# Performance work log

Hardware: AMD Instinct MI355X
Metric: run time of the kernel (lower is better)

## Reference

```python
import jax, jax.numpy as jnp
import numpy as np

N = 100_000   # nodes
E = 800_000   # edges
F_IN = 128    # num_features
E_IN = 64     # edge_dim
H = 100       # n_hidden
L = 2         # num_gnn_layers
BN_EPS = 1e-5


def _lin(key, fan_in, fan_out, extra=()):
    kw, _ = jax.random.split(key)
    w = jax.random.normal(kw, (*extra, fan_in, fan_out), jnp.float32) / np.float32(np.sqrt(fan_in))
    b = jnp.zeros((*extra, fan_out), jnp.float32)
    return w, b


def setup_inputs() -> dict:
    key = jax.random.key(0)
    ks = jax.random.split(key, 12)
    x = jax.random.normal(ks[0], (N, F_IN), jnp.float32)
    edge_index = jax.random.randint(ks[1], (2, E), 0, N, dtype=jnp.int32)
    edge_attr = jax.random.normal(ks[2], (E, E_IN), jnp.float32)
    node_w, node_b = _lin(ks[3], F_IN, H)
    edge_w, edge_b = _lin(ks[4], E_IN, H)
    lin_w, lin_b = _lin(ks[5], H, H, (L,))   # GINEConv edge lin per layer
    w1, b1 = _lin(ks[6], H, H, (L,))         # GINEConv nn first Linear
    w2, b2 = _lin(ks[7], H, H, (L,))         # GINEConv nn second Linear
    gamma = jnp.ones((L, H), jnp.float32)
    beta = jnp.zeros((L, H), jnp.float32)
    ew1, eb1 = _lin(ks[8], 3 * H, H, (L,))   # edge-update MLP
    ew2, eb2 = _lin(ks[9], H, H, (L,))
    mw1, mb1 = _lin(ks[10], 3 * H, 50)
    k11, k12 = jax.random.split(ks[11])
    mw2, mb2 = _lin(k11, 50, 25)
    mw3, mb3 = _lin(k12, 25, 2)
    return dict(x=x, edge_index=edge_index, edge_attr=edge_attr,
                node_w=node_w, node_b=node_b, edge_w=edge_w, edge_b=edge_b,
                lin_w=lin_w, lin_b=lin_b, w1=w1, b1=b1, w2=w2, b2=b2,
                gamma=gamma, beta=beta, ew1=ew1, eb1=eb1, ew2=ew2, eb2=eb2,
                mw1=mw1, mb1=mb1, mw2=mw2, mb2=mb2, mw3=mw3, mb3=mb3)


def reference(x, edge_index, edge_attr, node_w, node_b, edge_w, edge_b,
              lin_w, lin_b, w1, b1, w2, b2, gamma, beta,
              ew1, eb1, ew2, eb2, mw1, mb1, mw2, mb2, mw3, mb3):
    src, dst = edge_index[0], edge_index[1]
    h = x @ node_w + node_b          # [N, H]
    e = edge_attr @ edge_w + edge_b  # [E, H]
    for i in range(L):
        # GINEConv: message = relu(x_src + lin(edge_attr)); sum-aggregate at dst
        msg = jax.nn.relu(h[src] + (e @ lin_w[i] + lin_b[i]))       # [E, H]
        agg = jax.ops.segment_sum(msg, dst, num_segments=N)         # [N, H]
        z = h + agg                                                  # (1+eps)*x + aggr, eps=0
        z = jax.nn.relu(z @ w1[i] + b1[i]) @ w2[i] + b2[i]
        # BatchNorm over nodes (training mode, biased variance)
        mu = z.mean(0)
        var = z.var(0)
        z = (z - mu) * jax.lax.rsqrt(var + BN_EPS) * gamma[i] + beta[i]
        h = (h + jax.nn.relu(z)) / 2
        # edge update: emlp(cat(x_src, x_dst, e))
        cat = jnp.concatenate([h[src], h[dst], e], axis=-1)         # [E, 3H]
        e = e + (jax.nn.relu(cat @ ew1[i] + eb1[i]) @ ew2[i] + eb2[i]) / 2
    feat = jnp.concatenate(
        [jax.nn.relu(jnp.concatenate([h[src], h[dst]], axis=-1)), e], axis=1)  # [E, 3H]
    out = jax.nn.relu(feat @ mw1 + mb1)
    out = jax.nn.relu(out @ mw2 + mb2)
    return out @ mw3 + mb3  # [E, 2]
```

## Files before the change

kernel.cpp:

```cpp
#include <hip/hip_runtime.h>

#define N_NODES 100000
#define N_EDGES 800000
#define HDIM 100
#define LDP 112
#define TSTR 104

typedef __attribute__((ext_vector_type(8))) short bf16x8;
typedef __attribute__((ext_vector_type(4))) float f32x4;

__device__ inline uint packsplit(float v) {
    uint u = __float_as_uint(v);
    float r = v - __uint_as_float(u & 0xFFFF0000u);
    return (u & 0xFFFF0000u) | (__float_as_uint(r) >> 16);
}
__device__ inline float recw(uint w) {
    return __uint_as_float(w & 0xFFFF0000u) + __uint_as_float(w << 16);
}
__device__ inline uint4 relu4(uint4 a) {
    a.x &= ~(uint)((int)a.x >> 31); a.y &= ~(uint)((int)a.y >> 31);
    a.z &= ~(uint)((int)a.z >> 31); a.w &= ~(uint)((int)a.w >> 31);
    return a;
}
__device__ inline void unpack16(uint4 a, uint4 b, bf16x8& h8, bf16x8& l8) {
    union { uint u[4]; bf16x8 v; } H, L;
    H.u[0] = __builtin_amdgcn_perm(a.y, a.x, 0x07060302u);
    H.u[1] = __builtin_amdgcn_perm(a.w, a.z, 0x07060302u);
    H.u[2] = __builtin_amdgcn_perm(b.y, b.x, 0x07060302u);
    H.u[3] = __builtin_amdgcn_perm(b.w, b.z, 0x07060302u);
    L.u[0] = __builtin_amdgcn_perm(a.y, a.x, 0x05040100u);
    L.u[1] = __builtin_amdgcn_perm(a.w, a.z, 0x05040100u);
    L.u[2] = __builtin_amdgcn_perm(b.y, b.x, 0x05040100u);
    L.u[3] = __builtin_amdgcn_perm(b.w, b.z, 0x05040100u);
    h8 = H.v; l8 = L.v;
}
__device__ inline void split8(float4 a, float4 b, bf16x8& h8, bf16x8& l8) {
    float v[8] = {a.x, a.y, a.z, a.w, b.x, b.y, b.z, b.w};
    bf16x8 hh, ll;
#pragma unroll
    for (int i = 0; i < 8; ++i) {
        uint u = __float_as_uint(v[i]);
        hh[i] = (short)(u >> 16);
        float r = v[i] - __uint_as_float(u & 0xFFFF0000u);
        ll[i] = (short)(__float_as_uint(r) >> 16);
    }
    h8 = hh; l8 = ll;
}

template<int CONCAT>
__global__ __launch_bounds__(256)
void pack_k(const float* __restrict__ W, ushort* __restrict__ hi, ushort* __restrict__ lo,
            int K, int NC, int Kpad, int NCpad, int total)
{
    int idx = blockIdx.x * 256 + threadIdx.x;
    if (idx >= total) return;
    int per = NCpad * Kpad;
    int b = idx / per, rem = idx - b * per;
    int col = rem / Kpad, kv = rem - col * Kpad;
    int srck; bool valid;
    if (CONCAT) {
        int seg = kv >> 7, off = kv & 127;
        srck = seg * 100 + off;
        valid = (off < 100) && (srck < K) && (col < NC);
    } else {
        srck = kv;
        valid = (kv < K) && (col < NC);
    }
    float v = valid ? W[(long)b * K * NC + (long)srck * NC + col] : 0.f;
    uint w = packsplit(v);
    hi[idx] = (ushort)(w >> 16);
    lo[idx] = (ushort)(w & 0xFFFFu);
}

template<int TILES, int TPW, int STEPS, int MODE, int GATHER, int AFP32, int OUTF32, int CLAMP>
__global__ __launch_bounds__(256, 2)
void gemm9_k(const uint* aP, int lda, const float* __restrict__ aF, int ldaf,
             const ushort* __restrict__ wH, const ushort* __restrict__ wL,
             const float* __restrict__ bias,
             float* __restrict__ Cf, uint* cP, int ldc,
             int M, int NC, const int* __restrict__ g0)
{
    constexpr int KPADW = STEPS * 32;
    const int tid  = threadIdx.x;
    const int lane = tid & 63;
    const int w    = tid >> 6;
    const int cl   = lane & 15;
    const int kgrp = lane >> 4;
    const long row0 = (long)blockIdx.x * 64;

    int arows[4];
#pragma unroll
    for (int rg = 0; rg < 4; ++rg) {
        long grow = row0 + rg * 16 + cl;
        int gc = (int)((grow < M) ? grow : (M - 1));
        arows[rg] = (GATHER == 3) ? g0[gc] : gc;
    }

    uint4  aw0[2][4], aw1[2][4];
    float4 af0[2][4], af1[2][4];
    bf16x8 bh[2][TPW], bl[2][TPW];
    f32x4  acc[TPW][4];
#pragma unroll
    for (int tp = 0; tp < TPW; ++tp)
#pragma unroll
        for (int rg = 0; rg < 4; ++rg) acc[tp][rg] = (f32x4){0.f, 0.f, 0.f, 0.f};

    auto loadA = [&](int st, int sl) {
        const int kk = st * 32 + kgrp * 8;
#pragma unroll
        for (int rg = 0; rg < 4; ++rg) {
            if (AFP32) {
                const float* p = aF + (size_t)arows[rg] * ldaf + kk;
                af0[sl][rg] = *(const float4*)p;
                af1[sl][rg] = *(const float4*)(p + 4);
            } else {
                bool ok = !CLAMP || ((st & 3) != 3) || (kgrp == 0);
                if (ok) {
                    const uint* p = aP + (size_t)arows[rg] * lda + kk;
                    aw0[sl][rg] = *(const uint4*)p;
                    aw1[sl][rg] = *(const uint4*)(p + 4);
                } else {
                    aw0[sl][rg] = make_uint4(0, 0, 0, 0);
                    aw1[sl][rg] = make_uint4(0, 0, 0, 0);
                }
            }
        }
    };
    auto loadB = [&](int st, int sl) {
        int kk = st * 32 + kgrp * 8;
#pragma unroll
        for (int tp = 0; tp < TPW; ++tp) {
            int colw = (w * TPW + tp) * 16 + cl;
            bh[sl][tp] = *(const bf16x8*)(wH + (size_t)colw * KPADW + kk);
            bl[sl][tp] = *(const bf16x8*)(wL + (size_t)colw * KPADW + kk);
        }
    };

    loadA(0, 0); loadB(0, 0);
    if (STEPS > 1) { loadA(1, 1); loadB(1, 1); }

#pragma unroll
    for (int st = 0; st < STEPS; ++st) {
        const int sl = st & 1;
#pragma unroll
        for (int rg = 0; rg < 4; ++rg) {
            bf16x8 aH, aL;
            if (AFP32) split8(af0[sl][rg], af1[sl][rg], aH, aL);
            else       unpack16(aw0[sl][rg], aw1[sl][rg], aH, aL);
#pragma unroll
            for (int tp = 0; tp < TPW; ++tp) {
                acc[tp][rg] = __builtin_amdgcn_mfma_f32_16x16x32_bf16(aL, bh[sl][tp], acc[tp][rg], 0, 0, 0);
                acc[tp][rg] = __builtin_amdgcn_mfma_f32_16x16x32_bf16(aH, bl[sl][tp], acc[tp][rg], 0, 0, 0);
                acc[tp][rg] = __builtin_amdgcn_mfma_f32_16x16x32_bf16(aH, bh[sl][tp], acc[tp][rg], 0, 0, 0);
            }
        }
        if (st + 2 < STEPS) { loadA(st + 2, sl); loadB(st + 2, sl); }
    }

#pragma unroll
    for (int tp = 0; tp < TPW; ++tp) {
        int col = (w * TPW + tp) * 16 + cl;
        if (col >= NC) continue;
        float bv = bias[col];
#pragma unroll
        for (int rg = 0; rg < 4; ++rg) {
#pragma unroll
            for (int i = 0; i < 4; ++i) {
                long grow = row0 + rg * 16 + kgrp * 4 + i;
                if (grow >= M) continue;
                float v = acc[tp][rg][i] + bv;
                if (MODE == 1) v = fmaxf(v, 0.f);
                long o = grow * (long)ldc + col;
                if (OUTF32) Cf[o] = v;
                else        cP[o] = packsplit(v);
            }
        }
    }
}

__global__ __launch_bounds__(256, 2)
void msg_agg_k(const uint* __restrict__ eP,
               const ushort* __restrict__ wH, const ushort* __restrict__ wL,
               const float* __restrict__ bias,
               const uint* __restrict__ hP,
               const int* __restrict__ psrc, const int* __restrict__ pdst,
               float* __restrict__ aggF)
{
    __shared__ float sm[64 * 108];
    __shared__ int sd[64];
    const int tid = threadIdx.x, lane = tid & 63, w = tid >> 6;
    const int cl = lane & 15, kgrp = lane >> 4;
    const long row0 = (long)blockIdx.x * 64;

    if (tid < 64) sd[tid] = pdst[row0 + tid];

    int sr[4][4];
#pragma unroll
    for (int rg = 0; rg < 4; ++rg)
#pragma unroll
        for (int i = 0; i < 4; ++i)
            sr[rg][i] = psrc[row0 + rg * 16 + kgrp * 4 + i];

    uint4 aw0[2][4], aw1[2][4];
    bf16x8 bh[2][2], bl[2][2];
    f32x4 acc[2][4];
#pragma unroll
    for (int tp = 0; tp < 2; ++tp)
#pragma unroll
        for (int rg = 0; rg < 4; ++rg) acc[tp][rg] = (f32x4){0.f, 0.f, 0.f, 0.f};

    auto loadA = [&](int st, int sl) {
        const int kk = st * 32 + kgrp * 8;
        bool ok = ((st & 3) != 3) || (kgrp == 0);
#pragma unroll
        for (int rg = 0; rg < 4; ++rg) {
            if (ok) {
                const uint* p = eP + (size_t)(row0 + rg * 16 + cl) * LDP + kk;
                aw0[sl][rg] = *(const uint4*)p;
                aw1[sl][rg] = *(const uint4*)(p + 4);
            } else {
                aw0[sl][rg] = make_uint4(0, 0, 0, 0);
                aw1[sl][rg] = make_uint4(0, 0, 0, 0);
            }
        }
    };
    auto loadB = [&](int st, int sl) {
        int kk = st * 32 + kgrp * 8;
#pragma unroll
        for (int tp = 0; tp < 2; ++tp) {
            int colw = (w * 2 + tp) * 16 + cl;
            bh[sl][tp] = *(const bf16x8*)(wH + (size_t)colw * 128 + kk);
            bl[sl][tp] = *(const bf16x8*)(wL + (size_t)colw * 128 + kk);
        }
    };

    loadA(0, 0); loadB(0, 0); loadA(1, 1); loadB(1, 1);
#pragma unroll
    for (int st = 0; st < 4; ++st) {
        const int sl = st & 1;
#pragma unroll
        for (int rg = 0; rg < 4; ++rg) {
            bf16x8 aH, aL;
            unpack16(aw0[sl][rg], aw1[sl][rg], aH, aL);
#pragma unroll
            for (int tp = 0; tp < 2; ++tp) {
                acc[tp][rg] = __builtin_amdgcn_mfma_f32_16x16x32_bf16(aL, bh[sl][tp], acc[tp][rg], 0, 0, 0);
                acc[tp][rg] = __builtin_amdgcn_mfma_f32_16x16x32_bf16(aH, bl[sl][tp], acc[tp][rg], 0, 0, 0);
                acc[tp][rg] = __builtin_amdgcn_mfma_f32_16x16x32_bf16(aH, bh[sl][tp], acc[tp][rg], 0, 0, 0);
            }
        }
        if (st + 2 < 4) { loadA(st + 2, sl); loadB(st + 2, sl); }
    }

#pragma unroll
    for (int tp = 0; tp < 2; ++tp) {
        int col = (w * 2 + tp) * 16 + cl;
        if (col < 100) {
            float bv = bias[col];
#pragma unroll
            for (int rg = 0; rg < 4; ++rg)
#pragma unroll
                for (int i = 0; i < 4; ++i) {
                    int row = rg * 16 + kgrp * 4 + i;
                    float hv = recw(hP[(size_t)sr[rg][i] * LDP + col]);
                    sm[row * 108 + col] = fmaxf(acc[tp][rg][i] + bv + hv, 0.f);
                }
        }
    }
    __syncthreads();

    if (tid < 100) {
        const int c = tid;
        int cur = sd[0];
        float s = 0.f;
        bool first = true;
        for (int r = 0; r < 64; ++r) {
            int d = sd[r];
            if (d != cur) {
                bool contPrev = first && (row0 > 0) && (pdst[row0 - 1] == cur);
                if (contPrev) atomicAdd(&aggF[(size_t)cur * TSTR + c], s);
                else aggF[(size_t)cur * TSTR + c] = recw(hP[(size_t)cur * LDP + c]) + s;
                first = false; s = 0.f; cur = d;
            }
            s += sm[r * 108 + c];
        }
        bool contPrev = first && (row0 > 0) && (pdst[row0 - 1] == cur);
        bool contNext = (row0 + 64 < N_EDGES) && (pdst[row0 + 64] == cur);
        if (contPrev || contNext) atomicAdd(&aggF[(size_t)cur * TSTR + c], s);
        else aggF[(size_t)cur * TSTR + c] = recw(hP[(size_t)cur * LDP + c]) + s;
    }
}

__global__ __launch_bounds__(256, 2)
void fused_edge_k(const uint* __restrict__ hP, uint* eP,
                  const ushort* __restrict__ w1H, const ushort* __restrict__ w1L,
                  const float* __restrict__ b1v,
                  const ushort* __restrict__ w2H, const ushort* __restrict__ w2L,
                  const float* __restrict__ b2v,
                  const int* __restrict__ g0, const int* __restrict__ g1)
{
    __shared__ uint sm[64 * 108];
    const int tid = threadIdx.x, lane = tid & 63, w = tid >> 6;
    const int cl = lane & 15, kgrp = lane >> 4;
    const long row0 = (long)blockIdx.x * 64;

    int rs[4], rd[4];
#pragma unroll
    for (int rg = 0; rg < 4; ++rg) {
        long gr = row0 + rg * 16 + cl;
        rs[rg] = g0[gr]; rd[rg] = g1[gr];
    }

    uint4 aw0[2][4], aw1[2][4];
    bf16x8 bh[2][2], bl[2][2];
    f32x4 acc[2][4];
#pragma unroll
    for (int tp = 0; tp < 2; ++tp)
#pragma unroll
        for (int rg = 0; rg < 4; ++rg) acc[tp][rg] = (f32x4){0.f, 0.f, 0.f, 0.f};

    auto loadA = [&](int st, int sl) {
        int seg = st >> 2, inseg = (st & 3) * 32 + kgrp * 8;
        bool ok = ((st & 3) != 3) || (kgrp == 0);
        const uint* base = (seg == 2) ? eP : hP;
#pragma unroll
        for (int rg = 0; rg < 4; ++rg) {
            if (ok) {
                long row = (seg == 0) ? rs[rg] : (seg == 1) ? rd[rg] : (row0 + rg * 16 + cl);
                const uint* p = base + (size_t)row * LDP + inseg;
                aw0[sl][rg] = *(const uint4*)p;
                aw1[sl][rg] = *(const uint4*)(p + 4);
            } else {
                aw0[sl][rg] = make_uint4(0, 0, 0, 0);
                aw1[sl][rg] = make_uint4(0, 0, 0, 0);
            }
        }
    };
    auto loadB = [&](int st, int sl) {
        int kk = st * 32 + kgrp * 8;
#pragma unroll
        for (int tp = 0; tp < 2; ++tp) {
            int colw = (w * 2 + tp) * 16 + cl;
            bh[sl][tp] = *(const bf16x8*)(w1H + (size_t)colw * 384 + kk);
            bl[sl][tp] = *(const bf16x8*)(w1L + (size_t)colw * 384 + kk);
        }
    };

    loadA(0, 0); loadB(0, 0); loadA(1, 1); loadB(1, 1);
#pragma unroll
    for (int st = 0; st < 12; ++st) {
        const int sl = st & 1;
#pragma unroll
        for (int rg = 0; rg < 4; ++rg) {
            bf16x8 aH, aL;
            unpack16(aw0[sl][rg], aw1[sl][rg], aH, aL);
#pragma unroll
            for (int tp = 0; tp < 2; ++tp) {
                acc[tp][rg] = __builtin_amdgcn_mfma_f32_16x16x32_bf16(aL, bh[sl][tp], acc[tp][rg], 0, 0, 0);
                acc[tp][rg] = __builtin_amdgcn_mfma_f32_16x16x32_bf16(aH, bl[sl][tp], acc[tp][rg], 0, 0, 0);
                acc[tp][rg] = __builtin_amdgcn_mfma_f32_16x16x32_bf16(aH, bh[sl][tp], acc[tp][rg], 0, 0, 0);
            }
        }
        if (st + 2 < 12) { loadA(st + 2, sl); loadB(st + 2, sl); }
    }

#pragma unroll
    for (int tp = 0; tp < 2; ++tp) {
        int col = (w * 2 + tp) * 16 + cl;
        if (col < 108) {
            float bv = (col < 100) ? b1v[col] : 0.f;
#pragma unroll
            for (int rg = 0; rg < 4; ++rg)
#pragma unroll
                for (int i = 0; i < 4; ++i) {
                    int row = rg * 16 + kgrp * 4 + i;
                    uint u = 0;
                    if (col < 100) u = packsplit(fmaxf(acc[tp][rg][i] + bv, 0.f));
                    sm[row * 108 + col] = u;
                }
        }
    }
    __syncthreads();

    f32x4 acc2[2][4];
#pragma unroll
    for (int tp = 0; tp < 2; ++tp)
#pragma unroll
        for (int rg = 0; rg < 4; ++rg) acc2[tp][rg] = (f32x4){0.f, 0.f, 0.f, 0.f};
    bf16x8 ch[2][2], clo[2][2];
    auto loadB2 = [&](int st, int sl) {
        int kk = st * 32 + kgrp * 8;
#pragma unroll
        for (int tp = 0; tp < 2; ++tp) {
            int colw = (w * 2 + tp) * 16 + cl;
            ch[sl][tp]  = *(const bf16x8*)(w2H + (size_t)colw * 128 + kk);
            clo[sl][tp] = *(const bf16x8*)(w2L + (size_t)colw * 128 + kk);
        }
    };
    loadB2(0, 0); loadB2(1, 1);
#pragma unroll
    for (int st = 0; st < 4; ++st) {
        const int sl = st & 1;
#pragma unroll
        for (int rg = 0; rg < 4; ++rg) {
            int row = rg * 16 + cl;
            int kk = st * 32 + kgrp * 8;
            uint4 q0 = make_uint4(0, 0, 0, 0), q1 = make_uint4(0, 0, 0, 0);
            if ((st != 3) || (kgrp == 0)) {
                q0 = *(const uint4*)&sm[row * 108 + kk];
                q1 = *(const uint4*)&sm[row * 108 + kk + 4];
            }
            bf16x8 aH, aL;
            unpack16(q0, q1, aH, aL);
#pragma unroll
            for (int tp = 0; tp < 2; ++tp) {
                acc2[tp][rg] = __builtin_amdgcn_mfma_f32_16x16x32_bf16(aL, ch[sl][tp], acc2[tp][rg], 0, 0, 0);
                acc2[tp][rg] = __builtin_amdgcn_mfma_f32_16x16x32_bf16(aH, clo[sl][tp], acc2[tp][rg], 0, 0, 0);
                acc2[tp][rg] = __builtin_amdgcn_mfma_f32_16x16x32_bf16(aH, ch[sl][tp], acc2[tp][rg], 0, 0, 0);
            }
        }
        if (st + 2 < 4) loadB2(st + 2, sl);
    }
#pragma unroll
    for (int tp = 0; tp < 2; ++tp) {
        int col = (w * 2 + tp) * 16 + cl;
        if (col >= 100) continue;
        float bv = b2v[col];
#pragma unroll
        for (int rg = 0; rg < 4; ++rg)
#pragma unroll
            for (int i = 0; i < 4; ++i) {
                long grow = row0 + rg * 16 + kgrp * 4 + i;
                long o = grow * (long)LDP + col;
                float v = recw(eP[o]) + 0.5f * (acc2[tp][rg][i] + bv);
                eP[o] = packsplit(v);
            }
    }
}

__global__ __launch_bounds__(256, 2)
void fused_final_k(const uint* __restrict__ hP, const uint* __restrict__ eP,
                   const ushort* __restrict__ m1H, const ushort* __restrict__ m1L,
                   const float* __restrict__ mb1,
                   const ushort* __restrict__ m2H, const ushort* __restrict__ m2L,
                   const float* __restrict__ mb2, const float* __restrict__ mw3,
                   const float* __restrict__ mb3,
                   const int* __restrict__ g0, const int* __restrict__ g1,
                   const int* __restrict__ eidx, float* __restrict__ out)
{
    __shared__ uint sm[64 * 68];
    const int tid = threadIdx.x, lane = tid & 63, w = tid >> 6;
    const int cl = lane & 15, kgrp = lane >> 4;
    const long row0 = (long)blockIdx.x * 64;

    int rs[4], rd[4];
#pragma unroll
    for (int rg = 0; rg < 4; ++rg) {
        long gr = row0 + rg * 16 + cl;
        rs[rg] = g0[gr]; rd[rg] = g1[gr];
    }

    uint4 aw0[2][4], aw1[2][4];
    bf16x8 bh[2], bl[2];
    f32x4 acc1[4];
#pragma unroll
    for (int rg = 0; rg < 4; ++rg) acc1[rg] = (f32x4){0.f, 0.f, 0.f, 0.f};

    auto loadA = [&](int st, int sl) {
        int seg = st >> 2, inseg = (st & 3) * 32 + kgrp * 8;
        bool ok = ((st & 3) != 3) || (kgrp == 0);
        const uint* base = (seg == 2) ? eP : hP;
#pragma unroll
        for (int rg = 0; rg < 4; ++rg) {
            if (ok) {
                long row = (seg == 0) ? rs[rg] : (seg == 1) ? rd[rg] : (row0 + rg * 16 + cl);
                const uint* p = base + (size_t)row * LDP + inseg;
                aw0[sl][rg] = *(const uint4*)p;
                aw1[sl][rg] = *(const uint4*)(p + 4);
            } else {
                aw0[sl][rg] = make_uint4(0, 0, 0, 0);
                aw1[sl][rg] = make_uint4(0, 0, 0, 0);
            }
        }
    };
    auto loadB = [&](int st, int sl) {
        int kk = st * 32 + kgrp * 8;
        int colw = w * 16 + cl;
        bh[sl] = *(const bf16x8*)(m1H + (size_t)colw * 384 + kk);
        bl[sl] = *(const bf16x8*)(m1L + (size_t)colw * 384 + kk);
    };

    loadA(0, 0); loadB(0, 0); loadA(1, 1); loadB(1, 1);
#pragma unroll
    for (int st = 0; st < 12; ++st) {
        const int sl = st & 1;
#pragma unroll
        for (int rg = 0; rg < 4; ++rg) {
            uint4 w0 = aw0[sl][rg], w1 = aw1[sl][rg];
            if (st < 8) { w0 = relu4(w0); w1 = relu4(w1); }
            bf16x8 aH, aL;
            unpack16(w0, w1, aH, aL);
            acc1[rg] = __builtin_amdgcn_mfma_f32_16x16x32_bf16(aL, bh[sl], acc1[rg], 0, 0, 0);
            acc1[rg] = __builtin_amdgcn_mfma_f32_16x16x32_bf16(aH, bl[sl], acc1[rg], 0, 0, 0);
            acc1[rg] = __builtin_amdgcn_mfma_f32_16x16x32_bf16(aH, bh[sl], acc1[rg], 0, 0, 0);
        }
        if (st + 2 < 12) { loadA(st + 2, sl); loadB(st + 2, sl); }
    }

    {
        int col = w * 16 + cl;
        float bv = (col < 50) ? mb1[col] : 0.f;
#pragma unroll
        for (int rg = 0; rg < 4; ++rg)
#pragma unroll
            for (int i = 0; i < 4; ++i) {
                int row = rg * 16 + kgrp * 4 + i;
                uint u = 0;
                if (col < 50) u = packsplit(fmaxf(acc1[rg][i] + bv, 0.f));
                sm[row * 68 + col] = u;
            }
    }
    __syncthreads();

    bf16x8 c2h[2][2], c2l[2][2];
#pragma unroll
    for (int t = 0; t < 2; ++t)
#pragma unroll
        for (int st = 0; st < 2; ++st) {
            long o = (long)(t * 16 + cl) * 64 + st * 32 + kgrp * 8;
            c2h[t][st] = *(const bf16x8*)(m2H + o);
            c2l[t][st] = *(const bf16x8*)(m2L + o);
        }
    const float bias0 = mb2[cl];
    const float bias1 = (cl + 16 < 25) ? mb2[cl + 16] : 0.f;
    const float w3a0 = mw3[cl * 2 + 0], w3a1 = mw3[cl * 2 + 1];
    const float w3b0 = (cl + 16 < 25) ? mw3[(cl + 16) * 2 + 0] : 0.f;
    const float w3b1 = (cl + 16 < 25) ? mw3[(cl + 16) * 2 + 1] : 0.f;
    const float b30 = mb3[0], b31 = mb3[1];

    const int row = w * 16 + cl;
    f32x4 a0 = (f32x4){0.f, 0.f, 0.f, 0.f}, a1 = a0;
#pragma unroll
    for (int st = 0; st < 2; ++st) {
        int kk = st * 32 + kgrp * 8;
        uint4 q0 = *(const uint4*)&sm[row * 68 + kk];
        uint4 q1 = *(const uint4*)&sm[row * 68 + kk + 4];
        bf16x8 aH, aL;
        unpack16(q0, q1, aH, aL);
        a0 = __builtin_amdgcn_mfma_f32_16x16x32_bf16(aL, c2h[0][st], a0, 0, 0, 0);
        a0 = __builtin_amdgcn_mfma_f32_16x16x32_bf16(aH, c2l[0][st], a0, 0, 0, 0);
        a0 = __builtin_amdgcn_mfma_f32_16x16x32_bf16(aH, c2h[0][st], a0, 0, 0, 0);
        a1 = __builtin_amdgcn_mfma_f32_16x16x32_bf16(aL, c2h[1][st], a1, 0, 0, 0);
        a1 = __builtin_amdgcn_mfma_f32_16x16x32_bf16(aH, c2l[1][st], a1, 0, 0, 0);
        a1 = __builtin_amdgcn_mfma_f32_16x16x32_bf16(aH, c2h[1][st], a1, 0, 0, 0);
    }
#pragma unroll
    for (int i = 0; i < 4; ++i) {
        float t0 = fmaxf(a0[i] + bias0, 0.f);
        float t1 = fmaxf(a1[i] + bias1, 0.f);
        float s0 = t0 * w3a0 + t1 * w3b0;
        float s1 = t0 * w3a1 + t1 * w3b1;
#pragma unroll
        for (int d = 1; d < 16; d <<= 1) {
            s0 += __shfl_xor(s0, d, 64);
            s1 += __shfl_xor(s1, d, 64);
        }
        if (cl == 0) {
            long grow = row0 + w * 16 + kgrp * 4 + i;
            int oe = eidx[grow];
            out[(long)oe * 2 + 0] = s0 + b30;
            out[(long)oe * 2 + 1] = s1 + b31;
        }
    }
}

__global__ __launch_bounds__(256)
void hist_k(const int* __restrict__ dst, int* __restrict__ cnt)
{
    int e = blockIdx.x * 256 + threadIdx.x;
    if (e < N_EDGES) atomicAdd(&cnt[dst[e]], 1);
}

__global__ __launch_bounds__(1024)
void scan_k(const int* __restrict__ cnt, int* __restrict__ off)
{
    __shared__ int part[1024];
    const int t = threadIdx.x;
    const int per = (N_NODES + 1023) / 1024;
    const int base = t * per;
    int s = 0;
    for (int i = 0; i < per; ++i) {
        int n = base + i;
        if (n < N_NODES) s += cnt[n];
    }
    part[t] = s;
    __syncthreads();
    for (int d = 1; d < 1024; d <<= 1) {
        int v = (t >= d) ? part[t - d] : 0;
        __syncthreads();
        part[t] += v;
        __syncthreads();
    }
    int run = (t == 0) ? 0 : part[t - 1];
    for (int i = 0; i < per; ++i) {
        int n = base + i;
        if (n < N_NODES) { off[n] = run; run += cnt[n]; }
    }
    if (t == 1023) off[N_NODES] = run;
}

__global__ __launch_bounds__(256)
void fill_k(const int* __restrict__ dst, const int* __restrict__ off,
            int* __restrict__ pos, int* __restrict__ eidx)
{
    int e = blockIdx.x * 256 + threadIdx.x;
    if (e >= N_EDGES) return;
    int d = dst[e];
    int p = atomicAdd(&pos[d], 1);
    eidx[off[d] + p] = e;
}

__global__ __launch_bounds__(256)
void perm_k(const int* __restrict__ eidx, const int* __restrict__ src,
            const int* __restrict__ dst, int* __restrict__ psrc, int* __restrict__ pdst)
{
    int j = blockIdx.x * 256 + threadIdx.x;
    if (j >= N_EDGES) return;
    int e = eidx[j];
    psrc[j] = src[e];
    pdst[j] = dst[e];
}

__global__ __launch_bounds__(256)
void h2agg_k(const uint* __restrict__ hP, float* __restrict__ aggF)
{
    unsigned idx = blockIdx.x * 256u + threadIdx.x;
    if (idx >= (unsigned)(N_NODES * 26)) return;
    unsigned n = idx / 26u;
    unsigned q = (idx - n * 26u) * 4u;
    long ob = (long)n * TSTR + q;
    if (q >= 100) {
        *(float4*)&aggF[ob] = make_float4(0.f, 0.f, 0.f, 0.f);
        return;
    }
    uint4 hw = *(const uint4*)&hP[(long)n * LDP + q];
    *(float4*)&aggF[ob] = make_float4(recw(hw.x), recw(hw.y), recw(hw.z), recw(hw.w));
}

__global__ __launch_bounds__(128)
void bn_stats_k(const float* __restrict__ z, float* __restrict__ stats)
{
    int c = threadIdx.x;
    if (c >= HDIM) return;
    long rows_per = (N_NODES + gridDim.x - 1) / gridDim.x;
    long r0 = (long)blockIdx.x * rows_per;
    long r1 = r0 + rows_per; if (r1 > N_NODES) r1 = N_NODES;
    float s = 0.f, s2 = 0.f;
    for (long r = r0; r < r1; ++r) {
        float v = z[r * TSTR + c];
        s += v; s2 += v * v;
    }
    atomicAdd(&stats[c], s);
    atomicAdd(&stats[HDIM + c], s2);
}

__global__ __launch_bounds__(256)
void bn_apply_k(const float* __restrict__ z2, const float* __restrict__ stats,
                const float* __restrict__ gamma, const float* __restrict__ beta,
                uint* __restrict__ hP)
{
    unsigned idx = blockIdx.x * 256u + threadIdx.x;
    if (idx >= (unsigned)(N_NODES * 25)) return;
    unsigned n = idx / 25u;
    unsigned q = (idx - n * 25u) * 4u;
    const float invN = 1.f / N_NODES;
    long ob = (long)n * LDP + q;
    uint4 hw = *(const uint4*)&hP[ob];
    float4 zv = *(const float4*)&z2[(long)n * TSTR + q];
    float hv[4] = {recw(hw.x), recw(hw.y), recw(hw.z), recw(hw.w)};
    float zz[4] = {zv.x, zv.y, zv.z, zv.w};
    float r[4];
#pragma unroll
    for (int i = 0; i < 4; ++i) {
        unsigned c = q + i;
        float mu  = stats[c] * invN;
        float var = stats[HDIM + c] * invN - mu * mu;
        float v = (zz[i] - mu) * rsqrtf(var + 1e-5f) * gamma[c] + beta[c];
        r[i] = (hv[i] + fmaxf(v, 0.f)) * 0.5f;
    }
    *(uint4*)&hP[ob] = make_uint4(packsplit(r[0]), packsplit(r[1]), packsplit(r[2]), packsplit(r[3]));
}

static inline int gb64(long m) { return (int)((m + 63) / 64); }

extern "C" void kernel_launch(void* const* d_in, const int* in_sizes, int n_in,
                              void* d_out, int out_size, void* d_ws, size_t ws_size,
                              hipStream_t stream)
{
    const float* x         = (const float*)d_in[0];
    const int*   ei        = (const int*)  d_in[1];
    const float* edge_attr = (const float*)d_in[2];
    const float* node_w    = (const float*)d_in[3];
    const float* node_b    = (const float*)d_in[4];
    const float* edge_w    = (const float*)d_in[5];
    const float* edge_b    = (const float*)d_in[6];
    const float* lin_w     = (const float*)d_in[7];
    const float* lin_b     = (const float*)d_in[8];
    const float* w1        = (const float*)d_in[9];
    const float* b1        = (const float*)d_in[10];
    const float* w2        = (const float*)d_in[11];
    const float* b2        = (const float*)d_in[12];
    const float* gamma     = (const float*)d_in[13];
    const float* beta      = (const float*)d_in[14];
    const float* ew1       = (const float*)d_in[15];
    const float* eb1       = (const float*)d_in[16];
    const float* ew2       = (const float*)d_in[17];
    const float* eb2       = (const float*)d_in[18];
    const float* mw1       = (const float*)d_in[19];
    const float* mb1       = (const float*)d_in[20];
    const float* mw2       = (const float*)d_in[21];
    const float* mb2       = (const float*)d_in[22];
    const float* mw3       = (const float*)d_in[23];
    const float* mb3       = (const float*)d_in[24];
    float* out = (float*)d_out;

    ushort* pw = (ushort*)d_ws;
    size_t off_w = 0;
    ushort *nwH, *nwL, *ewH, *ewL, *liH, *liL, *w1H, *w1L, *w2H, *w2L,
           *e1H, *e1L, *e2H, *e2L, *m1H, *m1L, *m2H, *m2L;
    auto nextw = [&](size_t s, ushort*& H, ushort*& L) { H = pw + off_w; L = pw + off_w + s; off_w += 2 * s; };
    nextw(128 * 128,     nwH, nwL);
    nextw(128 * 64,      ewH, ewL);
    nextw(2 * 128 * 128, liH, liL);
    nextw(2 * 128 * 128, w1H, w1L);
    nextw(2 * 128 * 128, w2H, w2L);
    nextw(2 * 128 * 384, e1H, e1L);
    nextw(2 * 128 * 128, e2H, e2L);
    nextw(64 * 384,      m1H, m1L);
    nextw(32 * 64,       m2H, m2L);

    int* intb = (int*)((char*)d_ws + (2u << 20));
    int* cnt   = intb;
    int* coff  = cnt + N_NODES;
    int* pos   = coff + N_NODES + 1;
    int* eidx  = pos + N_NODES;
    int* psrc  = eidx + N_EDGES;
    int* pdst  = psrc + N_EDGES;
    float* stats = (float*)(pdst + N_EDGES);

    char* fbase = (char*)d_ws + (16u << 20);
    uint* eP = (uint*)fbase;
    uint* hP = eP + (size_t)N_EDGES * LDP;
    uint* zP = hP + (size_t)N_NODES * LDP;
    char* big = (char*)(zP + (size_t)N_NODES * LDP);
    float* aggF = (float*)big;
    float* z2   = aggF + (size_t)N_NODES * TSTR;

    const int* srcp = ei;
    const int* dstp = ei + N_EDGES;
    dim3 blk(256);

    auto packl = [&](const float* W, ushort* H, ushort* L, int K, int NC, int Kp, int NCp, int batch, bool cc) {
        int total = batch * NCp * Kp;
        if (cc) pack_k<1><<<(total + 255) / 256, blk, 0, stream>>>(W, H, L, K, NC, Kp, NCp, total);
        else    pack_k<0><<<(total + 255) / 256, blk, 0, stream>>>(W, H, L, K, NC, Kp, NCp, total);
    };
    packl(node_w, nwH, nwL, 128, 100, 128, 128, 1, false);
    packl(edge_w, ewH, ewL,  64, 100,  64, 128, 1, false);
    packl(lin_w,  liH, liL, 100, 100, 128, 128, 2, false);
    packl(w1,     w1H, w1L, 100, 100, 128, 128, 2, false);
    packl(w2,     w2H, w2L, 100, 100, 128, 128, 2, false);
    packl(ew1,    e1H, e1L, 300, 100, 384, 128, 2, true);
    packl(ew2,    e2H, e2L, 100, 100, 128, 128, 2, false);
    packl(mw1,    m1H, m1L, 300,  50, 384,  64, 1, true);
    packl(mw2,    m2H, m2L,  50,  25,  64,  32, 1, false);

    hipMemsetAsync(cnt, 0, N_NODES * sizeof(int), stream);
    hist_k<<<(N_EDGES + 255) / 256, blk, 0, stream>>>(dstp, cnt);
    scan_k<<<1, dim3(1024), 0, stream>>>(cnt, coff);
    hipMemsetAsync(pos, 0, N_NODES * sizeof(int), stream);
    fill_k<<<(N_EDGES + 255) / 256, blk, 0, stream>>>(dstp, coff, pos, eidx);
    perm_k<<<(N_EDGES + 255) / 256, blk, 0, stream>>>(eidx, srcp, dstp, psrc, pdst);

    gemm9_k<8,2,4,0,0,1,0,0><<<gb64(N_NODES), blk, 0, stream>>>(
        nullptr, 0, x, 128, nwH, nwL, node_b, nullptr, hP, LDP, N_NODES, 100, nullptr);
    gemm9_k<8,2,2,0,3,1,0,0><<<gb64(N_EDGES), blk, 0, stream>>>(
        nullptr, 0, edge_attr, 64, ewH, ewL, edge_b, nullptr, eP, LDP, N_EDGES, 100, eidx);

    for (int i = 0; i < 2; ++i) {
        h2agg_k<<<(N_NODES * 26 + 255) / 256, blk, 0, stream>>>(hP, aggF);
        msg_agg_k<<<gb64(N_EDGES), blk, 0, stream>>>(
            eP, liH + (size_t)i * 16384, liL + (size_t)i * 16384, lin_b + i * HDIM,
            hP, psrc, pdst, aggF);
        gemm9_k<8,2,4,1,0,1,0,0><<<gb64(N_NODES), blk, 0, stream>>>(
            nullptr, 0, aggF, TSTR, w1H + (size_t)i * 16384, w1L + (size_t)i * 16384,
            b1 + i * HDIM, nullptr, zP, LDP, N_NODES, 100, nullptr);
        gemm9_k<8,2,4,0,0,0,1,1><<<gb64(N_NODES), blk, 0, stream>>>(
            zP, LDP, nullptr, 0, w2H + (size_t)i * 16384, w2L + (size_t)i * 16384,
            b2 + i * HDIM, z2, nullptr, TSTR, N_NODES, 100, nullptr);
        hipMemsetAsync(stats, 0, 2 * HDIM * sizeof(float), stream);
        bn_stats_k<<<1024, dim3(128), 0, stream>>>(z2, stats);
        bn_apply_k<<<(N_NODES * 25 + 255) / 256, blk, 0, stream>>>(
            z2, stats, gamma + i * HDIM, beta + i * HDIM, hP);
        fused_edge_k<<<gb64(N_EDGES), blk, 0, stream>>>(
            hP, eP,
            e1H + (size_t)i * 49152, e1L + (size_t)i * 49152, eb1 + i * HDIM,
            e2H + (size_t)i * 16384, e2L + (size_t)i * 16384, eb2 + i * HDIM,
            psrc, pdst);
    }

    fused_final_k<<<gb64(N_EDGES), blk, 0, stream>>>(
        hP, eP, m1H, m1L, mb1, m2H, m2L, mb2, mw3, mb3, psrc, pdst, eidx, out);
}
```

Baseline: 3.550 ms.

## Stage gathered node rows into LDS via async global_load_lds in edge kernels

The three edge kernels (message aggregation, edge update, final MLP) now gather the 64 src and dst node rows per block into shared memory with asynchronous global-to-LDS loads at kernel start, instead of doing per-lane indirect global loads inside the MFMA k-loop. The GEMM is reordered to run the contiguous edge-feature segment first, overlapping the gather, and then the node segments are read from LDS. This aims to hide the random-gather latency and coalesce the row fetches. In exchange, LDS use per block grows (about 55KB per block in the two-table kernels), which may cut occupancy below the two blocks per CU requested by the launch bounds, and extra barriers are added.

```diff
diff --git a/kernel.cpp b/kernel.cpp
--- a/kernel.cpp
+++ b/kernel.cpp
@@ -5,6 +5,7 @@
 #define HDIM 100
 #define LDP 112
 #define TSTR 104
+#define TS 108
 
 typedef __attribute__((ext_vector_type(8))) short bf16x8;
 typedef __attribute__((ext_vector_type(4))) float f32x4;
@@ -45,6 +46,20 @@
         ll[i] = (short)(__float_as_uint(r) >> 16);
     }
     h8 = hh; l8 = ll;
+}
+
+__device__ inline void stage_rows(const uint* __restrict__ base, const int* rows,
+                                  uint* lds, int w, int lane)
+{
+    typedef __attribute__((address_space(1))) const uint GU;
+    typedef __attribute__((address_space(3))) uint LU;
+    for (int j = w; j < 27; j += 4) {
+        int chunk = j * 64 + lane;
+        int r = chunk / 27;
+        int c = chunk - r * 27;
+        const uint* g = base + (size_t)rows[r] * LDP + c * 4;
+        __builtin_amdgcn_global_load_lds((GU*)g, (LU*)(lds + j * 256), 16, 0, 0);
+    }
 }
 
 template<int CONCAT>
@@ -186,20 +201,16 @@
                const int* __restrict__ psrc, const int* __restrict__ pdst,
                float* __restrict__ aggF)
 {
-    __shared__ float sm[64 * 108];
-    __shared__ int sd[64];
+    __shared__ float sm[64 * TS];
+    __shared__ uint  t0[64 * TS];
+    __shared__ int sd[64], ssr[64];
     const int tid = threadIdx.x, lane = tid & 63, w = tid >> 6;
     const int cl = lane & 15, kgrp = lane >> 4;
     const long row0 = (long)blockIdx.x * 64;
 
-    if (tid < 64) sd[tid] = pdst[row0 + tid];
-
-    int sr[4][4];
-#pragma unroll
-    for (int rg = 0; rg < 4; ++rg)
-#pragma unroll
-        for (int i = 0; i < 4; ++i)
-            sr[rg][i] = psrc[row0 + rg * 16 + kgrp * 4 + i];
+    if (tid < 64) { sd[tid] = pdst[row0 + tid]; ssr[tid] = psrc[row0 + tid]; }
+    __syncthreads();
+    stage_rows(hP, ssr, t0, w, lane);
 
     uint4 aw0[2][4], aw1[2][4];
     bf16x8 bh[2][2], bl[2][2];
@@ -211,7 +222,7 @@
 
     auto loadA = [&](int st, int sl) {
         const int kk = st * 32 + kgrp * 8;
-        bool ok = ((st & 3) != 3) || (kgrp == 0);
+        bool ok = (st != 3) || (kgrp == 0);
 #pragma unroll
         for (int rg = 0; rg < 4; ++rg) {
             if (ok) {
@@ -251,6 +262,7 @@
         }
         if (st + 2 < 4) { loadA(st + 2, sl); loadB(st + 2, sl); }
     }
+    __syncthreads();
 
 #pragma unroll
     for (int tp = 0; tp < 2; ++tp) {
@@ -262,8 +274,8 @@
 #pragma unroll
                 for (int i = 0; i < 4; ++i) {
                     int row = rg * 16 + kgrp * 4 + i;
-                    float hv = recw(hP[(size_t)sr[rg][i] * LDP + col]);
-                    sm[row * 108 + col] = fmaxf(acc[tp][rg][i] + bv + hv, 0.f);
+                    float hv = recw(t0[row * TS + col]);
+                    sm[row * TS + col] = fmaxf(acc[tp][rg][i] + bv + hv, 0.f);
                 }
         }
     }
@@ -282,7 +294,7 @@
                 else aggF[(size_t)cur * TSTR + c] = recw(hP[(size_t)cur * LDP + c]) + s;
                 first = false; s = 0.f; cur = d;
             }
-            s += sm[r * 108 + c];
+            s += sm[r * TS + c];
         }
         bool contPrev = first && (row0 > 0) && (pdst[row0 - 1] == cur);
         bool contNext = (row0 + 64 < N_EDGES) && (pdst[row0 + 64] == cur);
@@ -299,17 +311,17 @@
                   const float* __restrict__ b2v,
                   const int* __restrict__ g0, const int* __restrict__ g1)
 {
-    __shared__ uint sm[64 * 108];
+    __shared__ uint t0[64 * TS];
+    __shared__ uint t1[64 * TS];
+    __shared__ int sidx[64], didx[64];
     const int tid = threadIdx.x, lane = tid & 63, w = tid >> 6;
     const int cl = lane & 15, kgrp = lane >> 4;
     const long row0 = (long)blockIdx.x * 64;
 
-    int rs[4], rd[4];
-#pragma unroll
-    for (int rg = 0; rg < 4; ++rg) {
-        long gr = row0 + rg * 16 + cl;
-        rs[rg] = g0[gr]; rd[rg] = g1[gr];
-    }
+    if (tid < 64) { sidx[tid] = g0[row0 + tid]; didx[tid] = g1[row0 + tid]; }
+    __syncthreads();
+    stage_rows(hP, sidx, t0, w, lane);
+    stage_rows(hP, didx, t1, w, lane);
 
     uint4 aw0[2][4], aw1[2][4];
     bf16x8 bh[2][2], bl[2][2];
@@ -319,15 +331,22 @@
 #pragma unroll
         for (int rg = 0; rg < 4; ++rg) acc[tp][rg] = (f32x4){0.f, 0.f, 0.f, 0.f};
 
-    auto loadA = [&](int st, int sl) {
-        int seg = st >> 2, inseg = (st & 3) * 32 + kgrp * 8;
-        bool ok = ((st & 3) != 3) || (kgrp == 0);
-        const uint* base = (seg == 2) ? eP : hP;
+    auto loadBk = [&](int kkbase, int st, int sl) {
+        int kk = kkbase + st * 32 + kgrp * 8;
+#pragma unroll
+        for (int tp = 0; tp < 2; ++tp) {
+            int colw = (w * 2 + tp) * 16 + cl;
+            bh[sl][tp] = *(const bf16x8*)(w1H + (size_t)colw * 384 + kk);
+            bl[sl][tp] = *(const bf16x8*)(w1L + (size_t)colw * 384 + kk);
+        }
+    };
+    auto loadAe = [&](int st, int sl) {
+        const int kk = st * 32 + kgrp * 8;
+        bool ok = (st != 3) || (kgrp == 0);
 #pragma unroll
         for (int rg = 0; rg < 4; ++rg) {
             if (ok) {
-                long row = (seg == 0) ? rs[rg] : (seg == 1) ? rd[rg] : (row0 + rg * 16 + cl);
-                const uint* p = base + (size_t)row * LDP + inseg;
+                const uint* p = eP + (size_t)(row0 + rg * 16 + cl) * LDP + kk;
                 aw0[sl][rg] = *(const uint4*)p;
                 aw1[sl][rg] = *(const uint4*)(p + 4);
             } else {
@@ -336,19 +355,10 @@
             }
         }
     };
-    auto loadB = [&](int st, int sl) {
-        int kk = st * 32 + kgrp * 8;
-#pragma unroll
-        for (int tp = 0; tp < 2; ++tp) {
-            int colw = (w * 2 + tp) * 16 + cl;
-            bh[sl][tp] = *(const bf16x8*)(w1H + (size_t)colw * 384 + kk);
-            bl[sl][tp] = *(const bf16x8*)(w1L + (size_t)colw * 384 + kk);
-        }
-    };
-
-    loadA(0, 0); loadB(0, 0); loadA(1, 1); loadB(1, 1);
-#pragma unroll
-    for (int st = 0; st < 12; ++st) {
+
+    loadAe(0, 0); loadBk(256, 0, 0); loadAe(1, 1); loadBk(256, 1, 1);
+#pragma unroll
+    for (int st = 0; st < 4; ++st) {
         const int sl = st & 1;
 #pragma unroll
         for (int rg = 0; rg < 4; ++rg) {
@@ -361,13 +371,45 @@
                 acc[tp][rg] = __builtin_amdgcn_mfma_f32_16x16x32_bf16(aH, bh[sl][tp], acc[tp][rg], 0, 0, 0);
             }
         }
-        if (st + 2 < 12) { loadA(st + 2, sl); loadB(st + 2, sl); }
-    }
+        if (st + 2 < 4) { loadAe(st + 2, sl); loadBk(256, st + 2, sl); }
+    }
+    __syncthreads();
+
+    loadBk(0, 0, 0); loadBk(0, 1, 1);
+#pragma unroll
+    for (int p = 0; p < 8; ++p) {
+        const int sl = p & 1;
+        const uint* t = (p < 4) ? t0 : t1;
+        int inseg = (p & 3) * 32 + kgrp * 8;
+        bool ok = ((p & 3) != 3) || (kgrp == 0);
+#pragma unroll
+        for (int rg = 0; rg < 4; ++rg) {
+            uint4 q0 = make_uint4(0, 0, 0, 0), q1 = make_uint4(0, 0, 0, 0);
+            if (ok) {
+                int ro = (rg * 16 + cl) * TS + inseg;
+                q0 = *(const uint4*)&t[ro];
+                q1 = *(const uint4*)&t[ro + 4];
+            }
+            bf16x8 aH, aL;
+            unpack16(q0, q1, aH, aL);
+#pragma unroll
+            for (int tp = 0; tp < 2; ++tp) {
+                acc[tp][rg] = __builtin_amdgcn_mfma_f32_16x16x32_bf16(aL, bh[sl][tp], acc[tp][rg], 0, 0, 0);
+                acc[tp][rg] = __builtin_amdgcn_mfma_f32_16x16x32_bf16(aH, bl[sl][tp], acc[tp][rg], 0, 0, 0);
+                acc[tp][rg] = __builtin_amdgcn_mfma_f32_16x16x32_bf16(aH, bh[sl][tp], acc[tp][rg], 0, 0, 0);
+            }
+        }
+        if (p + 2 < 8) {
+            int np = p + 2;
+            loadBk((np < 4) ? 0 : 128, np & 3, sl);
+        }
+    }
+    __syncthreads();
 
 #pragma unroll
     for (int tp = 0; tp < 2; ++tp) {
         int col = (w * 2 + tp) * 16 + cl;
-        if (col < 108) {
+        if (col < TS) {
             float bv = (col < 100) ? b1v[col] : 0.f;
 #pragma unroll
             for (int rg = 0; rg < 4; ++rg)
@@ -376,7 +418,7 @@
                     int row = rg * 16 + kgrp * 4 + i;
                     uint u = 0;
                     if (col < 100) u = packsplit(fmaxf(acc[tp][rg][i] + bv, 0.f));
-                    sm[row * 108 + col] = u;
+                    t0[row * TS + col] = u;
                 }
         }
     }
@@ -403,12 +445,12 @@
         const int sl = st & 1;
 #pragma unroll
         for (int rg = 0; rg < 4; ++rg) {
-            int row = rg * 16 + cl;
             int kk = st * 32 + kgrp * 8;
             uint4 q0 = make_uint4(0, 0, 0, 0), q1 = make_uint4(0, 0, 0, 0);
             if ((st != 3) || (kgrp == 0)) {
-                q0 = *(const uint4*)&sm[row * 108 + kk];
-                q1 = *(const uint4*)&sm[row * 108 + kk + 4];
+                int ro = (rg * 16 + cl) * TS + kk;
+                q0 = *(const uint4*)&t0[ro];
+                q1 = *(const uint4*)&t0[ro + 4];
             }
             bf16x8 aH, aL;
             unpack16(q0, q1, aH, aL);
@@ -448,17 +490,17 @@
                    const int* __restrict__ g0, const int* __restrict__ g1,
                    const int* __restrict__ eidx, float* __restrict__ out)
 {
-    __shared__ uint sm[64 * 68];
+    __shared__ uint t0[64 * TS];
+    __shared__ uint t1[64 * TS];
+    __shared__ int sidx[64], didx[64];
     const int tid = threadIdx.x, lane = tid & 63, w = tid >> 6;
     const int cl = lane & 15, kgrp = lane >> 4;
     const long row0 = (long)blockIdx.x * 64;
 
-    int rs[4], rd[4];
-#pragma unroll
-    for (int rg = 0; rg < 4; ++rg) {
-        long gr = row0 + rg * 16 + cl;
-        rs[rg] = g0[gr]; rd[rg] = g1[gr];
-    }
+    if (tid < 64) { sidx[tid] = g0[row0 + tid]; didx[tid] = g1[row0 + tid]; }
+    __syncthreads();
+    stage_rows(hP, sidx, t0, w, lane);
+    stage_rows(hP, didx, t1, w, lane);
 
     uint4 aw0[2][4], aw1[2][4];
     bf16x8 bh[2], bl[2];
@@ -466,15 +508,19 @@
 #pragma unroll
     for (int rg = 0; rg < 4; ++rg) acc1[rg] = (f32x4){0.f, 0.f, 0.f, 0.f};
 
-    auto loadA = [&](int st, int sl) {
-        int seg = st >> 2, inseg = (st & 3) * 32 + kgrp * 8;
-        bool ok = ((st & 3) != 3) || (kgrp == 0);
-        const uint* base = (seg == 2) ? eP : hP;
+    auto loadBk = [&](int kkbase, int st, int sl) {
+        int kk = kkbase + st * 32 + kgrp * 8;
+        int colw = w * 16 + cl;
+        bh[sl] = *(const bf16x8*)(m1H + (size_t)colw * 384 + kk);
+        bl[sl] = *(const bf16x8*)(m1L + (size_t)colw * 384 + kk);
+    };
+    auto loadAe = [&](int st, int sl) {
+        const int kk = st * 32 + kgrp * 8;
+        bool ok = (st != 3) || (kgrp == 0);
 #pragma unroll
         for (int rg = 0; rg < 4; ++rg) {
             if (ok) {
-                long row = (seg == 0) ? rs[rg] : (seg == 1) ? rd[rg] : (row0 + rg * 16 + cl);
-                const uint* p = base + (size_t)row * LDP + inseg;
+                const uint* p = eP + (size_t)(row0 + rg * 16 + cl) * LDP + kk;
                 aw0[sl][rg] = *(const uint4*)p;
                 aw1[sl][rg] = *(const uint4*)(p + 4);
             } else {
@@ -483,29 +529,50 @@
             }
         }
     };
-    auto loadB = [&](int st, int sl) {
-        int kk = st * 32 + kgrp * 8;
-        int colw = w * 16 + cl;
-        bh[sl] = *(const bf16x8*)(m1H + (size_t)colw * 384 + kk);
-        bl[sl] = *(const bf16x8*)(m1L + (size_t)colw * 384 + kk);
-    };
-
-    loadA(0, 0); loadB(0, 0); loadA(1, 1); loadB(1, 1);
-#pragma unroll
-    for (int st = 0; st < 12; ++st) {
+
+    loadAe(0, 0); loadBk(256, 0, 0); loadAe(1, 1); loadBk(256, 1, 1);
+#pragma unroll
+    for (int st = 0; st < 4; ++st) {
         const int sl = st & 1;
 #pragma unroll
         for (int rg = 0; rg < 4; ++rg) {
-            uint4 w0 = aw0[sl][rg], w1 = aw1[sl][rg];
-            if (st < 8) { w0 = relu4(w0); w1 = relu4(w1); }
             bf16x8 aH, aL;
-            unpack16(w0, w1, aH, aL);
+            unpack16(aw0[sl][rg], aw1[sl][rg], aH, aL);
             acc1[rg] = __builtin_amdgcn_mfma_f32_16x16x32_bf16(aL, bh[sl], acc1[rg], 0, 0, 0);
             acc1[rg] = __builtin_amdgcn_mfma_f32_16x16x32_bf16(aH, bl[sl], acc1[rg], 0, 0, 0);
             acc1[rg] = __builtin_amdgcn_mfma_f32_16x16x32_bf16(aH, bh[sl], acc1[rg], 0, 0, 0);
         }
-        if (st + 2 < 12) { loadA(st + 2, sl); loadB(st + 2, sl); }
-    }
+        if (st + 2 < 4) { loadAe(st + 2, sl); loadBk(256, st + 2, sl); }
+    }
+    __syncthreads();
+
+    loadBk(0, 0, 0); loadBk(0, 1, 1);
+#pragma unroll
+    for (int p = 0; p < 8; ++p) {
+        const int sl = p & 1;
+        const uint* t = (p < 4) ? t0 : t1;
+        int inseg = (p & 3) * 32 + kgrp * 8;
+        bool ok = ((p & 3) != 3) || (kgrp == 0);
+#pragma unroll
+        for (int rg = 0; rg < 4; ++rg) {
+            uint4 q0 = make_uint4(0, 0, 0, 0), q1 = make_uint4(0, 0, 0, 0);
+            if (ok) {
+                int ro = (rg * 16 + cl) * TS + inseg;
+                q0 = relu4(*(const uint4*)&t[ro]);
+                q1 = relu4(*(const uint4*)&t[ro + 4]);
+            }
+            bf16x8 aH, aL;
+            unpack16(q0, q1, aH, aL);
+            acc1[rg] = __builtin_amdgcn_mfma_f32_16x16x32_bf16(aL, bh[sl], acc1[rg], 0, 0, 0);
+            acc1[rg] = __builtin_amdgcn_mfma_f32_16x16x32_bf16(aH, bl[sl], acc1[rg], 0, 0, 0);
+            acc1[rg] = __builtin_amdgcn_mfma_f32_16x16x32_bf16(aH, bh[sl], acc1[rg], 0, 0, 0);
+        }
+        if (p + 2 < 8) {
+            int np = p + 2;
+            loadBk((np < 4) ? 0 : 128, np & 3, sl);
+        }
+    }
+    __syncthreads();
 
     {
         int col = w * 16 + cl;
@@ -517,7 +584,7 @@
                 int row = rg * 16 + kgrp * 4 + i;
                 uint u = 0;
                 if (col < 50) u = packsplit(fmaxf(acc1[rg][i] + bv, 0.f));
-                sm[row * 68 + col] = u;
+                t0[row * 68 + col] = u;
             }
     }
     __syncthreads();
@@ -543,8 +610,8 @@
 #pragma unroll
     for (int st = 0; st < 2; ++st) {
         int kk = st * 32 + kgrp * 8;
-        uint4 q0 = *(const uint4*)&sm[row * 68 + kk];
-        uint4 q1 = *(const uint4*)&sm[row * 68 + kk + 4];
+        uint4 q0 = *(const uint4*)&t0[row * 68 + kk];
+        uint4 q1 = *(const uint4*)&t0[row * 68 + kk + 4];
         bf16x8 aH, aL;
         unpack16(q0, q1, aH, aL);
         a0 = __builtin_amdgcn_mfma_f32_16x16x32_bf16(aL, c2h[0][st], a0, 0, 0, 0);
@@ -556,10 +623,10 @@
     }
 #pragma unroll
     for (int i = 0; i < 4; ++i) {
-        float t0 = fmaxf(a0[i] + bias0, 0.f);
-        float t1 = fmaxf(a1[i] + bias1, 0.f);
-        float s0 = t0 * w3a0 + t1 * w3b0;
-        float s1 = t0 * w3a1 + t1 * w3b1;
+        float t0v = fmaxf(a0[i] + bias0, 0.f);
+        float t1v = fmaxf(a1[i] + bias1, 0.f);
+        float s0 = t0v * w3a0 + t1v * w3b0;
+        float s1 = t0v * w3a1 + t1v * w3b1;
 #pragma unroll
         for (int d = 1; d < 16; d <<= 1) {
             s0 += __shfl_xor(s0, d, 64);
```

Result: slower. 3.653 ms (+2.9%).
